# Kernel optimization log

Hardware: AMD Instinct MI355X
Metric: run time of the kernel (lower is better)

The kernel has to match this reference:

```python
import jax, jax.numpy as jnp
import numpy as np

NH, NKV, HD = 16, 4, 64   # n_heads, n_kv_heads, head_dim
N_REP = NH // NKV
EPS = 1e-6


def rms_norm(x, w):
    var = jnp.mean(x.astype(jnp.float32) ** 2, axis=-1, keepdims=True)
    return (x.astype(jnp.float32) * jax.lax.rsqrt(var + EPS)).astype(x.dtype) * w


def rotate_half(x):
    x1, x2 = jnp.split(x, 2, axis=-1)
    return jnp.concatenate([-x2, x1], axis=-1)


def setup_inputs() -> dict:
    key = jax.random.key(0)
    ks = jax.random.split(key, 6)
    B, S, H = 2, 2048, 2048
    x = jax.random.normal(ks[0], (B, S, H), dtype=jnp.float32)
    # RoPE tables [S, HD]
    inv_freq = 1.0 / (10000.0 ** (jnp.arange(0, HD, 2, dtype=jnp.float32) / HD))
    freqs = jnp.arange(S, dtype=jnp.float32)[:, None] * inv_freq[None, :]
    emb = jnp.concatenate([freqs, freqs], axis=-1)
    cos, sin = jnp.cos(emb), jnp.sin(emb)
    scale = 0.02
    wq = jax.random.normal(ks[1], (H, NH * HD), dtype=jnp.float32) * scale
    wk = jax.random.normal(ks[2], (H, NKV * HD), dtype=jnp.float32) * scale
    wv = jax.random.normal(ks[3], (H, NKV * HD), dtype=jnp.float32) * scale
    wo = jax.random.normal(ks[4], (NH * HD, H), dtype=jnp.float32) * scale
    q_norm_w = jnp.ones((HD,), dtype=jnp.float32)
    k_norm_w = jnp.ones((HD,), dtype=jnp.float32)
    return {"x": x, "cos": cos, "sin": sin, "wq": wq, "wk": wk, "wv": wv,
            "wo": wo, "q_norm_w": q_norm_w, "k_norm_w": k_norm_w}


def reference(x, cos, sin, wq, wk, wv, wo, q_norm_w, k_norm_w):
    B, S, H = x.shape
    # QKV projections + per-head RMSNorm on q/k
    q = rms_norm((x @ wq).reshape(B, S, NH, HD), q_norm_w)
    k = rms_norm((x @ wk).reshape(B, S, NKV, HD), k_norm_w)
    v = (x @ wv).reshape(B, S, NKV, HD)
    # RoPE (broadcast over heads)
    c = cos[None, :S, None, :]
    s = sin[None, :S, None, :]
    q = q * c + rotate_half(q) * s
    k = k * c + rotate_half(k) * s
    # prefill with S == window_size: no KV eviction, T == S -> causal mask
    k = jnp.repeat(k, N_REP, axis=2)  # [B,S,NH,HD]
    v = jnp.repeat(v, N_REP, axis=2)
    scores = jnp.einsum('bqhd,bkhd->bhqk', q, k) / jnp.sqrt(jnp.float32(HD))
    causal = jnp.triu(jnp.full((S, S), -jnp.inf, dtype=scores.dtype), 1)
    scores = scores + causal
    attn = jax.nn.softmax(scores.astype(jnp.float32), axis=-1).astype(q.dtype)
    out = jnp.einsum('bhqk,bkhd->bqhd', attn, v).reshape(B, S, NH * HD)
    return out @ wo
```

## Files before the change

### kernel.cpp

```cpp
#include <hip/hip_runtime.h>

typedef float floatx4 __attribute__((ext_vector_type(4)));
typedef __bf16 bfx8 __attribute__((ext_vector_type(8)));
typedef __bf16 bfx4 __attribute__((ext_vector_type(4)));

constexpr int B_ = 2, S_ = 2048, H_ = 2048, NH_ = 16, NKV_ = 4, HD_ = 64;
constexpr int M_ = B_ * S_;
constexpr int NQKV_ = NH_ * HD_ + 2 * NKV_ * HD_;
constexpr int HQ_ = NH_ * HD_;
constexpr int XP_ = 2056;
constexpr int AP_ = 1032;
constexpr int VP_ = 2056;
constexpr int QKV_ELEMS_ = M_ * NQKV_;

#define GLB(p) ((const __attribute__((address_space(1))) void*)(p))
#define LDS(p) ((__attribute__((address_space(3))) void*)(p))

__global__ __launch_bounds__(256) void prep_kernel(const float* __restrict__ x,
                                                   const float* __restrict__ wq,
                                                   const float* __restrict__ wk,
                                                   const float* __restrict__ wv,
                                                   const float* __restrict__ wo,
                                                   __bf16* __restrict__ xbf,
                                                   __bf16* __restrict__ wqkvT,
                                                   __bf16* __restrict__ woT) {
  __shared__ float tile[32][33];
  int bid = blockIdx.x;
  if (bid < M_) {
    const float4* s = (const float4*)(x + (size_t)bid * H_);
    __bf16* d = xbf + (size_t)bid * XP_;
#pragma unroll
    for (int i = 0; i < 2; i++) {
      int c = i * 256 + threadIdx.x;
      float4 v = s[c];
      bfx4 o;
      o[0] = (__bf16)v.x; o[1] = (__bf16)v.y; o[2] = (__bf16)v.z; o[3] = (__bf16)v.w;
      *(bfx4*)(d + c * 4) = o;
    }
    return;
  }
  bid -= M_;
  const float* src; __bf16* dst; int N, dstOff, pitch, nbx;
  if (bid < 2048)      { src = wq; dst = wqkvT; N = 1024; dstOff = 0;    pitch = XP_; nbx = 32; }
  else if (bid < 2560) { bid -= 2048; src = wk; dst = wqkvT; N = 256; dstOff = 1024; pitch = XP_; nbx = 8; }
  else if (bid < 3072) { bid -= 2560; src = wv; dst = wqkvT; N = 256; dstOff = 1280; pitch = XP_; nbx = 8; }
  else                 { bid -= 3072; src = wo; dst = woT;   N = 2048; dstOff = 0;   pitch = AP_; nbx = 64; }
  int n0 = (bid % nbx) * 32, k0 = (bid / nbx) * 32;
  int tx = threadIdx.x & 31, ty = threadIdx.x >> 5;
#pragma unroll
  for (int r = 0; r < 32; r += 8)
    tile[ty + r][tx] = src[(size_t)(k0 + ty + r) * N + n0 + tx];
  __syncthreads();
#pragma unroll
  for (int r = 0; r < 32; r += 8)
    dst[(size_t)(n0 + ty + r + dstOff) * pitch + k0 + tx] = (__bf16)tile[tx][ty + r];
}

__global__ __launch_bounds__(512) void gemm_bf16_f32(const __bf16* __restrict__ A,
                                                     const __bf16* __restrict__ Bt,
                                                     float* __restrict__ C,
                                                     int M, int N, int K,
                                                     int lda, int ldb, int ldc,
                                                     unsigned long long cstride) {
  __shared__ __align__(16) __bf16 As[256 * 64];
  __shared__ __align__(16) __bf16 Bs[128 * 64];
  int wid = threadIdx.x >> 6, lane = threadIdx.x & 63;
  int l15 = lane & 15, quad = lane >> 4;
  int wm = (wid >> 1) * 64, wn = (wid & 1) * 64;
  int m0 = blockIdx.y * 256, n0 = blockIdx.x * 128;
  int kb0 = blockIdx.z * K;
  C += (size_t)blockIdx.z * cstride;
  int srow_off = lane >> 3;
  int gphys = lane & 7;
  floatx4 acc[4][4] = {};
  for (int kb = kb0; kb < kb0 + K; kb += 64) {
#pragma unroll
    for (int j = 0; j < 4; j++) {
      int rbase = j * 64 + wid * 8;
      int row = rbase + srow_off;
      int glog = gphys ^ (row & 7);
      const __bf16* ga = &A[(size_t)(m0 + row) * lda + kb + glog * 8];
      __builtin_amdgcn_global_load_lds(GLB(ga), LDS(&As[rbase * 64]), 16, 0, 0);
    }
#pragma unroll
    for (int j = 0; j < 2; j++) {
      int rbase = j * 64 + wid * 8;
      int row = rbase + srow_off;
      int glog = gphys ^ (row & 7);
      const __bf16* gb = &Bt[(size_t)(n0 + row) * ldb + kb + glog * 8];
      __builtin_amdgcn_global_load_lds(GLB(gb), LDS(&Bs[rbase * 64]), 16, 0, 0);
    }
    __syncthreads();
#pragma unroll
    for (int kk = 0; kk < 64; kk += 32) {
      int cgq = (kk >> 3) + quad;
      bfx8 af[4], bfr[4];
#pragma unroll
      for (int mi = 0; mi < 4; mi++) {
        int row = wm + mi * 16 + l15;
        af[mi] = *(const bfx8*)&As[row * 64 + (cgq ^ (row & 7)) * 8];
      }
#pragma unroll
      for (int ni = 0; ni < 4; ni++) {
        int row = wn + ni * 16 + l15;
        bfr[ni] = *(const bfx8*)&Bs[row * 64 + (cgq ^ (row & 7)) * 8];
      }
#pragma unroll
      for (int mi = 0; mi < 4; mi++)
#pragma unroll
        for (int ni = 0; ni < 4; ni++)
          acc[mi][ni] = __builtin_amdgcn_mfma_f32_16x16x32_bf16(af[mi], bfr[ni], acc[mi][ni], 0, 0, 0);
    }
    __syncthreads();
  }
#pragma unroll
  for (int mi = 0; mi < 4; mi++)
#pragma unroll
    for (int ni = 0; ni < 4; ni++) {
      int row = m0 + wm + mi * 16 + quad * 4;
      int coln = n0 + wn + ni * 16 + l15;
#pragma unroll
      for (int r = 0; r < 4; r++)
        C[(size_t)(row + r) * ldc + coln] = acc[mi][ni][r];
    }
}

__global__ __launch_bounds__(256) void norm_rope_kernel(const float* __restrict__ qkv,
                                                        const float* __restrict__ cosT,
                                                        const float* __restrict__ sinT,
                                                        const float* __restrict__ qw,
                                                        const float* __restrict__ kw,
                                                        __bf16* __restrict__ Qo,
                                                        __bf16* __restrict__ Ko,
                                                        __bf16* __restrict__ VTo) {
  int s = blockIdx.x, b = blockIdx.y;
  int wid = threadIdx.x >> 6, lane = threadIdx.x & 63;
  const float* rowp = qkv + (size_t)(b * S_ + s) * NQKV_;
  const float* rowp2 = rowp + QKV_ELEMS_;
  float c = cosT[s * HD_ + lane];
  float sn = sinT[s * HD_ + lane];
#pragma unroll
  for (int it = 0; it < 5; it++) {
    int hh = it * 4 + wid;
    int idx = hh * 64 + lane;
    float v = rowp[idx] + rowp2[idx];
    float ss = v * v;
#pragma unroll
    for (int off = 1; off < 64; off <<= 1) ss += __shfl_xor(ss, off);
    float rs = rsqrtf(ss * (1.0f / 64.0f) + 1e-6f);
    const float* w = (hh < 16) ? qw : kw;
    float nv = v * rs * w[lane];
    float other = __shfl_xor(nv, 32);
    float rot = (lane < 32) ? -other : other;
    float outv = nv * c + rot * sn;
    if (hh < 16)
      Qo[(((size_t)b * NH_ + hh) * S_ + s) * HD_ + lane] = (__bf16)outv;
    else
      Ko[(((size_t)b * NKV_ + (hh - 16)) * S_ + s) * HD_ + lane] = (__bf16)outv;
  }
  {
    int idx = (20 + wid) * 64 + lane;
    float v = rowp[idx] + rowp2[idx];
    VTo[(((size_t)b * NKV_ + wid) * HD_ + lane) * VP_ + s] = (__bf16)v;
  }
}

__global__ __launch_bounds__(256, 4) void attn_kernel(const __bf16* __restrict__ Q,
                                                      const __bf16* __restrict__ Kc,
                                                      const __bf16* __restrict__ VT,
                                                      __bf16* __restrict__ Ob) {
  int px = blockIdx.x, h = blockIdx.y, b = blockIdx.z;
  int u = (px + 2 * (h & 7)) & 31;
  int qt = (((h >> 3) ^ b) & 1) ? (31 - u) : u;
  int wid = threadIdx.x >> 6, lane = threadIdx.x & 63;
  int l15 = lane & 15, quad = lane >> 4;
  int q0 = qt * 64 + wid * 16;
  int kvh = h >> 2;
  const __bf16* Qh = Q + (((size_t)b * NH_ + h) * S_ + q0) * HD_;
  const __bf16* Kh = Kc + ((size_t)b * NKV_ + kvh) * S_ * HD_;
  const __bf16* Vh = VT + ((size_t)b * NKV_ + kvh) * (size_t)HD_ * VP_;
  __shared__ __align__(16) __bf16 Ks[64][72];
  __shared__ __align__(16) __bf16 Vs[64][72];
  __shared__ __align__(16) __bf16 Pst[4][16][72];
  __bf16 (*P)[72] = Pst[wid];

  int srow = threadIdx.x >> 3;
  int scol = (threadIdx.x & 7) * 8;

  bfx8 qf0, qf1;
  {
    const __bf16* qp = Qh + l15 * HD_ + quad * 8;
    qf0 = *(const bfx8*)qp;
    qf1 = *(const bfx8*)(qp + 32);
  }
  floatx4 oacc[4] = {};
  float ps = 0.f;
  int ntiles = qt + 1;
  bfx8 kpre0, kpre1, vpre0, vpre1;
  kpre0 = *(const bfx8*)&Kh[(size_t)srow * HD_ + scol];
  kpre1 = *(const bfx8*)&Kh[(size_t)(srow + 32) * HD_ + scol];
  vpre0 = *(const bfx8*)&Vh[(size_t)srow * VP_ + scol];
  vpre1 = *(const bfx8*)&Vh[(size_t)(srow + 32) * VP_ + scol];
  for (int kt = 0; kt < ntiles; kt++) {
    int kv0 = kt * 64;
    int dq = q0 - kv0;
    __syncthreads();
    *(bfx8*)&Ks[srow][scol] = kpre0;
    *(bfx8*)&Ks[srow + 32][scol] = kpre1;
    *(bfx8*)&Vs[srow][scol] = vpre0;
    *(bfx8*)&Vs[srow + 32][scol] = vpre1;
    __syncthreads();
    if (kt + 1 < ntiles) {
      int kn = kv0 + 64;
      kpre0 = *(const bfx8*)&Kh[(size_t)(kn + srow) * HD_ + scol];
      kpre1 = *(const bfx8*)&Kh[(size_t)(kn + srow + 32) * HD_ + scol];
      vpre0 = *(const bfx8*)&Vh[(size_t)srow * VP_ + kn + scol];
      vpre1 = *(const bfx8*)&Vh[(size_t)(srow + 32) * VP_ + kn + scol];
    }
    floatx4 sf[4];
#pragma unroll
    for (int nt = 0; nt < 4; nt++) {
      bfx8 kf0 = *(const bfx8*)&Ks[nt * 16 + l15][quad * 8];
      bfx8 kf1 = *(const bfx8*)&Ks[nt * 16 + l15][32 + quad * 8];
      floatx4 z = {0.f, 0.f, 0.f, 0.f};
      z = __builtin_amdgcn_mfma_f32_16x16x32_bf16(kf0, qf0, z, 0, 0, 0);
      sf[nt] = __builtin_amdgcn_mfma_f32_16x16x32_bf16(kf1, qf1, z, 0, 0, 0);
    }
#pragma unroll
    for (int nt = 0; nt < 4; nt++) {
      bfx4 pk;
#pragma unroll
      for (int r = 0; r < 4; r++) {
        int kvrel = nt * 16 + quad * 4 + r;
        float p = __expf(sf[nt][r] * 0.125f);
        p = (kvrel - l15 > dq) ? 0.f : p;
        ps += p;
        pk[r] = (__bf16)p;
      }
      *(bfx4*)&P[l15][nt * 16 + quad * 4] = pk;
    }
    bfx8 pa0 = *(const bfx8*)&P[l15][quad * 8];
    bfx8 pa1 = *(const bfx8*)&P[l15][32 + quad * 8];
#pragma unroll
    for (int ot = 0; ot < 4; ot++) {
      bfx8 vf0 = *(const bfx8*)&Vs[ot * 16 + l15][quad * 8];
      bfx8 vf1 = *(const bfx8*)&Vs[ot * 16 + l15][32 + quad * 8];
      oacc[ot] = __builtin_amdgcn_mfma_f32_16x16x32_bf16(pa0, vf0, oacc[ot], 0, 0, 0);
      oacc[ot] = __builtin_amdgcn_mfma_f32_16x16x32_bf16(pa1, vf1, oacc[ot], 0, 0, 0);
    }
  }
  ps += __shfl_xor(ps, 16);
  ps += __shfl_xor(ps, 32);
  float rl[4];
#pragma unroll
  for (int r = 0; r < 4; r++) rl[r] = 1.0f / __shfl(ps, quad * 4 + r);
#pragma unroll
  for (int ot = 0; ot < 4; ot++)
#pragma unroll
    for (int r = 0; r < 4; r++) {
      float val = oacc[ot][r] * rl[r];
      Ob[((size_t)b * S_ + q0 + quad * 4 + r) * AP_ + h * HD_ + ot * 16 + l15] = (__bf16)val;
    }
}

extern "C" void kernel_launch(void* const* d_in, const int* in_sizes, int n_in,
                              void* d_out, int out_size, void* d_ws, size_t ws_size,
                              hipStream_t stream) {
  const float* x   = (const float*)d_in[0];
  const float* cosT = (const float*)d_in[1];
  const float* sinT = (const float*)d_in[2];
  const float* wq  = (const float*)d_in[3];
  const float* wk  = (const float*)d_in[4];
  const float* wv  = (const float*)d_in[5];
  const float* wo  = (const float*)d_in[6];
  const float* qw  = (const float*)d_in[7];
  const float* kw  = (const float*)d_in[8];
  float* out = (float*)d_out;

  char* w = (char*)d_ws;
  __bf16* xbf   = (__bf16*)(w);
  __bf16* wqkvT = (__bf16*)(w + 16842752);
  __bf16* woT   = (__bf16*)(w + 23158784);
  float*  qkv   = (float*) (w + 27385856);
  __bf16* attnO = (__bf16*)(w + 27385856);
  __bf16* Qb    = (__bf16*)(w + 77717504);
  __bf16* Kb    = (__bf16*)(w + 86106112);
  __bf16* VTb   = (__bf16*)(w + 88203264);

  prep_kernel<<<M_ + 5120, 256, 0, stream>>>(x, wq, wk, wv, wo, xbf, wqkvT, woT);
  gemm_bf16_f32<<<dim3(NQKV_ / 128, M_ / 256, 2), 512, 0, stream>>>(
      xbf, wqkvT, qkv, M_, NQKV_, H_ / 2, XP_, XP_, NQKV_, (unsigned long long)QKV_ELEMS_);
  norm_rope_kernel<<<dim3(S_, B_), 256, 0, stream>>>(qkv, cosT, sinT, qw, kw, Qb, Kb, VTb);
  attn_kernel<<<dim3(32, NH_, B_), 256, 0, stream>>>(Qb, Kb, VTb, attnO);
  gemm_bf16_f32<<<dim3(H_ / 128, M_ / 256, 1), 512, 0, stream>>>(
      attnO, woT, out, M_, H_, HQ_, AP_, AP_, H_, 0ull);
}
```

Baseline: 235.1 us.

## Double-buffer attention K/V with direct global-to-LDS loads and 128-row query tiles

The attention kernel now uses 512-thread blocks covering 128 query rows, which doubles reuse of each K/V tile loaded into shared memory. K/V tiles are double-buffered and loaded with global_load_lds into an XOR-swizzled layout, removing the register staging step and one barrier per iteration. Unmasked tiles skip the causal mask check, and exp is replaced by exp2 with a folded scale. Waves whose rows end early still wait at barriers until the block's last tile, and the grid now has half as many blocks, which may hurt occupancy or load balance.

```diff
diff --git a/kernel.cpp b/kernel.cpp
--- a/kernel.cpp
+++ b/kernel.cpp
@@ -165,27 +165,30 @@
   }
 }
 
-__global__ __launch_bounds__(256, 4) void attn_kernel(const __bf16* __restrict__ Q,
+__global__ __launch_bounds__(512, 4) void attn_kernel(const __bf16* __restrict__ Q,
                                                       const __bf16* __restrict__ Kc,
                                                       const __bf16* __restrict__ VT,
                                                       __bf16* __restrict__ Ob) {
   int px = blockIdx.x, h = blockIdx.y, b = blockIdx.z;
-  int u = (px + 2 * (h & 7)) & 31;
-  int qt = (((h >> 3) ^ b) & 1) ? (31 - u) : u;
+  int u = (px + 2 * (h & 7)) & 15;
+  int qt = (((h >> 3) ^ b) & 1) ? (15 - u) : u;
   int wid = threadIdx.x >> 6, lane = threadIdx.x & 63;
   int l15 = lane & 15, quad = lane >> 4;
-  int q0 = qt * 64 + wid * 16;
+  int q0w = qt * 128 + wid * 16;
   int kvh = h >> 2;
-  const __bf16* Qh = Q + (((size_t)b * NH_ + h) * S_ + q0) * HD_;
+  const __bf16* Qh = Q + (((size_t)b * NH_ + h) * S_ + q0w) * HD_;
   const __bf16* Kh = Kc + ((size_t)b * NKV_ + kvh) * S_ * HD_;
   const __bf16* Vh = VT + ((size_t)b * NKV_ + kvh) * (size_t)HD_ * VP_;
-  __shared__ __align__(16) __bf16 Ks[64][72];
-  __shared__ __align__(16) __bf16 Vs[64][72];
-  __shared__ __align__(16) __bf16 Pst[4][16][72];
+  __shared__ __align__(16) __bf16 Ks2[2][64 * 64];
+  __shared__ __align__(16) __bf16 Vs2[2][64 * 64];
+  __shared__ __align__(16) __bf16 Pst[8][16][72];
   __bf16 (*P)[72] = Pst[wid];
 
-  int srow = threadIdx.x >> 3;
-  int scol = (threadIdx.x & 7) * 8;
+  int srow = wid * 8 + (lane >> 3);
+  int gph = (lane & 7) ^ (srow & 7);
+  const __bf16* gK = Kh + (size_t)srow * HD_ + gph * 8;
+  const __bf16* gV = Vh + (size_t)srow * VP_ + gph * 8;
+  int ldsOff = wid * 8 * 64;
 
   bfx8 qf0, qf1;
   {
@@ -195,56 +198,72 @@
   }
   floatx4 oacc[4] = {};
   float ps = 0.f;
-  int ntiles = qt + 1;
-  bfx8 kpre0, kpre1, vpre0, vpre1;
-  kpre0 = *(const bfx8*)&Kh[(size_t)srow * HD_ + scol];
-  kpre1 = *(const bfx8*)&Kh[(size_t)(srow + 32) * HD_ + scol];
-  vpre0 = *(const bfx8*)&Vh[(size_t)srow * VP_ + scol];
-  vpre1 = *(const bfx8*)&Vh[(size_t)(srow + 32) * VP_ + scol];
+  int ntiles = 2 * qt + 2;
+  int ktmask = q0w >> 6;
+  constexpr float SCL = 0.125f * 1.44269504088896340736f;
+
+  __builtin_amdgcn_global_load_lds(GLB(gK), LDS(&Ks2[0][ldsOff]), 16, 0, 0);
+  __builtin_amdgcn_global_load_lds(GLB(gV), LDS(&Vs2[0][ldsOff]), 16, 0, 0);
+
   for (int kt = 0; kt < ntiles; kt++) {
-    int kv0 = kt * 64;
-    int dq = q0 - kv0;
-    __syncthreads();
-    *(bfx8*)&Ks[srow][scol] = kpre0;
-    *(bfx8*)&Ks[srow + 32][scol] = kpre1;
-    *(bfx8*)&Vs[srow][scol] = vpre0;
-    *(bfx8*)&Vs[srow + 32][scol] = vpre1;
+    int buf = kt & 1;
     __syncthreads();
     if (kt + 1 < ntiles) {
-      int kn = kv0 + 64;
-      kpre0 = *(const bfx8*)&Kh[(size_t)(kn + srow) * HD_ + scol];
-      kpre1 = *(const bfx8*)&Kh[(size_t)(kn + srow + 32) * HD_ + scol];
-      vpre0 = *(const bfx8*)&Vh[(size_t)srow * VP_ + kn + scol];
-      vpre1 = *(const bfx8*)&Vh[(size_t)(srow + 32) * VP_ + kn + scol];
-    }
+      int kn = (kt + 1) * 64;
+      __builtin_amdgcn_global_load_lds(GLB(gK + (size_t)kn * HD_), LDS(&Ks2[buf ^ 1][ldsOff]), 16, 0, 0);
+      __builtin_amdgcn_global_load_lds(GLB(gV + kn), LDS(&Vs2[buf ^ 1][ldsOff]), 16, 0, 0);
+    }
+    if (kt > ktmask) continue;
+
+    const __bf16* Ksb = Ks2[buf];
+    const __bf16* Vsb = Vs2[buf];
     floatx4 sf[4];
 #pragma unroll
     for (int nt = 0; nt < 4; nt++) {
-      bfx8 kf0 = *(const bfx8*)&Ks[nt * 16 + l15][quad * 8];
-      bfx8 kf1 = *(const bfx8*)&Ks[nt * 16 + l15][32 + quad * 8];
+      int r = nt * 16 + l15;
+      int pg = (quad ^ (r & 7)) * 8;
+      bfx8 kf0 = *(const bfx8*)&Ksb[r * 64 + pg];
+      bfx8 kf1 = *(const bfx8*)&Ksb[r * 64 + (pg ^ 32)];
       floatx4 z = {0.f, 0.f, 0.f, 0.f};
       z = __builtin_amdgcn_mfma_f32_16x16x32_bf16(kf0, qf0, z, 0, 0, 0);
       sf[nt] = __builtin_amdgcn_mfma_f32_16x16x32_bf16(kf1, qf1, z, 0, 0, 0);
     }
-#pragma unroll
-    for (int nt = 0; nt < 4; nt++) {
-      bfx4 pk;
-#pragma unroll
-      for (int r = 0; r < 4; r++) {
-        int kvrel = nt * 16 + quad * 4 + r;
-        float p = __expf(sf[nt][r] * 0.125f);
-        p = (kvrel - l15 > dq) ? 0.f : p;
-        ps += p;
-        pk[r] = (__bf16)p;
+    if (kt < ktmask) {
+#pragma unroll
+      for (int nt = 0; nt < 4; nt++) {
+        bfx4 pk;
+#pragma unroll
+        for (int r = 0; r < 4; r++) {
+          float p = exp2f(sf[nt][r] * SCL);
+          ps += p;
+          pk[r] = (__bf16)p;
+        }
+        *(bfx4*)&P[l15][nt * 16 + quad * 4] = pk;
       }
-      *(bfx4*)&P[l15][nt * 16 + quad * 4] = pk;
+    } else {
+      int dq = q0w - kt * 64;
+#pragma unroll
+      for (int nt = 0; nt < 4; nt++) {
+        bfx4 pk;
+#pragma unroll
+        for (int r = 0; r < 4; r++) {
+          int kvrel = nt * 16 + quad * 4 + r;
+          float p = exp2f(sf[nt][r] * SCL);
+          p = (kvrel - l15 > dq) ? 0.f : p;
+          ps += p;
+          pk[r] = (__bf16)p;
+        }
+        *(bfx4*)&P[l15][nt * 16 + quad * 4] = pk;
+      }
     }
     bfx8 pa0 = *(const bfx8*)&P[l15][quad * 8];
     bfx8 pa1 = *(const bfx8*)&P[l15][32 + quad * 8];
 #pragma unroll
     for (int ot = 0; ot < 4; ot++) {
-      bfx8 vf0 = *(const bfx8*)&Vs[ot * 16 + l15][quad * 8];
-      bfx8 vf1 = *(const bfx8*)&Vs[ot * 16 + l15][32 + quad * 8];
+      int d = ot * 16 + l15;
+      int vg = (quad ^ (d & 7)) * 8;
+      bfx8 vf0 = *(const bfx8*)&Vsb[d * 64 + vg];
+      bfx8 vf1 = *(const bfx8*)&Vsb[d * 64 + (vg ^ 32)];
       oacc[ot] = __builtin_amdgcn_mfma_f32_16x16x32_bf16(pa0, vf0, oacc[ot], 0, 0, 0);
       oacc[ot] = __builtin_amdgcn_mfma_f32_16x16x32_bf16(pa1, vf1, oacc[ot], 0, 0, 0);
     }
@@ -259,7 +278,7 @@
 #pragma unroll
     for (int r = 0; r < 4; r++) {
       float val = oacc[ot][r] * rl[r];
-      Ob[((size_t)b * S_ + q0 + quad * 4 + r) * AP_ + h * HD_ + ot * 16 + l15] = (__bf16)val;
+      Ob[((size_t)b * S_ + q0w + quad * 4 + r) * AP_ + h * HD_ + ot * 16 + l15] = (__bf16)val;
     }
 }
 
@@ -291,7 +310,7 @@
   gemm_bf16_f32<<<dim3(NQKV_ / 128, M_ / 256, 2), 512, 0, stream>>>(
       xbf, wqkvT, qkv, M_, NQKV_, H_ / 2, XP_, XP_, NQKV_, (unsigned long long)QKV_ELEMS_);
   norm_rope_kernel<<<dim3(S_, B_), 256, 0, stream>>>(qkv, cosT, sinT, qw, kw, Qb, Kb, VTb);
-  attn_kernel<<<dim3(32, NH_, B_), 256, 0, stream>>>(Qb, Kb, VTb, attnO);
+  attn_kernel<<<dim3(S_ / 128, NH_, B_), 512, 0, stream>>>(Qb, Kb, VTb, attnO);
   gemm_bf16_f32<<<dim3(H_ / 128, M_ / 256, 1), 512, 0, stream>>>(
       attnO, woT, out, M_, H_, HQ_, AP_, AP_, H_, 0ull);
 }
```

Measured after the change: 241.0 us. 1.03x slower.
